# Performance work log

Hardware: AMD Instinct MI355X
Metric: run time of the kernel (lower is better)

## Reference

```python
import jax, jax.numpy as jnp
import numpy as np

H = 768; I = 3072; NH = 12; HD = H // NH; L = 2; V = 32000
N = 2048; NSUB = 8; SUBLEN = 256; WIDTH = 512; EPS = 1e-6


def rmsnorm(x, w):
    x32 = x.astype(jnp.float32)
    n = x32 * jax.lax.rsqrt(jnp.mean(x32 * x32, axis=-1, keepdims=True) + EPS)
    return (n * w).astype(x.dtype)


def fixed_pos_embedding(ages, dim):
    # inv_freq: [dim//2]; torch.linspace(0, 2, steps=dim//2)
    inv_freq = 1.0 / (10000.0 ** jnp.linspace(0.0, 2.0, dim // 2))
    t = ages[:, None] * inv_freq[None, :]              # [N, dim//2]
    # stack((s, s), -1).reshape -> duplicate each entry pairwise (interleaved)
    sin = jnp.repeat(jnp.sin(t), 2, axis=-1)[:, None, :]  # [N, 1, dim]
    cos = jnp.repeat(jnp.cos(t), 2, axis=-1)[:, None, :]
    return sin, cos


def apply_rope(x, sin, cos):
    # x: [N, heads, hd]; sin/cos: [N, 1, hd]
    x1 = x[..., 0::2]
    x2 = x[..., 1::2]
    rot = jnp.stack((-x2, x1), axis=-1).reshape(x.shape)
    return x * cos + rot * sin


def build_mask(subject_lengths, n):
    # block-diagonal (per subject) + causal local window of WIDTH
    csum = jnp.cumsum(subject_lengths)
    idx = jnp.arange(n)
    seg = jnp.searchsorted(csum, idx, side='right')   # subject id per token
    i = idx[:, None]; j = idx[None, :]
    same = seg[:, None] == seg[None, :]
    return same & (j <= i) & ((i - j) < WIDTH)        # [N, N] bool


def encoder_layer(x, time_data, sin, cos, mask, norm_w, W_in, W_out):
    h = rmsnorm(x, norm_w)
    all_time = jnp.concatenate((time_data, time_data ** 2), axis=-1)  # [N, 4]
    h = h.at[:, -all_time.shape[1]:].set(all_time.astype(h.dtype))
    t = h @ W_in                                      # [N, 2I + 3H]
    ff = t[:, : 2 * I]
    qkv = t[:, 2 * I:].reshape(-1, 3, NH, HD)
    q = apply_rope(qkv[:, 0], sin, cos)
    k = apply_rope(qkv[:, 1], sin, cos)
    v = qkv[:, 2]
    scores = jnp.einsum('qhd,khd->hqk', q, k) / jnp.sqrt(jnp.float32(HD))
    scores = jnp.where(mask[None, :, :], scores, -jnp.inf)
    probs = jax.nn.softmax(scores, axis=-1)
    attn = jnp.einsum('hqk,khd->qhd', probs, v).reshape(-1, H)
    x1, x2 = jnp.split(ff, 2, axis=-1)
    ffo = jax.nn.silu(x1) * x2                        # swiglu
    return jnp.concatenate((attn, ffo), axis=-1) @ W_out


def setup_inputs() -> dict:
    key = jax.random.key(0)
    ks = jax.random.split(key, 6)
    tokens = jax.random.randint(ks[0], (N,), 0, V)
    ages = jnp.sort(jax.random.uniform(ks[1], (N,), dtype=jnp.float32) * 100.0)
    time_data = jax.random.normal(ks[2], (N, 2), dtype=jnp.float32)
    subject_lengths = jnp.full((NSUB,), SUBLEN, dtype=jnp.int32)
    embed_table = jax.random.normal(ks[3], (V, H), dtype=jnp.float32) * 0.02
    in_norm_w = jnp.ones((H,), jnp.float32)
    out_norm_w = jnp.ones((H,), jnp.float32)
    layer_norm_w = jnp.ones((L, H), jnp.float32)
    layer_Win = jax.random.normal(ks[4], (L, H, 2 * I + 3 * H), dtype=jnp.float32) / np.sqrt(H)
    layer_Wout = jax.random.normal(ks[5], (L, H + I, H), dtype=jnp.float32) / np.sqrt(H + I)
    return dict(tokens=tokens, ages=ages, time_data=time_data,
                subject_lengths=subject_lengths, embed_table=embed_table,
                in_norm_w=in_norm_w, out_norm_w=out_norm_w,
                layer_norm_w=layer_norm_w, layer_Win=layer_Win, layer_Wout=layer_Wout)


def reference(tokens, ages, time_data, subject_lengths, embed_table,
              in_norm_w, out_norm_w, layer_norm_w, layer_Win, layer_Wout):
    x = embed_table[tokens]                           # [N, H]
    x = rmsnorm(x, in_norm_w)
    sin, cos = fixed_pos_embedding(ages, HD)
    mask = build_mask(subject_lengths, x.shape[0])
    for l in range(L):
        x = x + encoder_layer(x, time_data, sin, cos, mask,
                              layer_norm_w[l], layer_Win[l], layer_Wout[l])
    return rmsnorm(x, out_norm_w)
```

## Files before the change

### kernel.cpp

```cpp
#include <hip/hip_runtime.h>
#include <math.h>

typedef unsigned short ushort_t;
typedef float f32x4 __attribute__((ext_vector_type(4)));
typedef __bf16 bf16x8 __attribute__((ext_vector_type(8)));

#define DEVFN __device__ __forceinline__

DEVFN ushort_t f2bf(float f) {
  unsigned int u = __float_as_uint(f);
  u += 0x7FFFu + ((u >> 16) & 1u);
  return (ushort_t)(u >> 16);
}
DEVFN float bf2f(ushort_t u) { return __uint_as_float((unsigned int)u << 16); }

DEVFN void gload(const ushort_t* src, char* dst) {
  __builtin_amdgcn_global_load_lds(
      (const __attribute__((address_space(1))) unsigned int*)src,
      (__attribute__((address_space(3))) unsigned int*)dst, 16, 0, 0);
}

#define N_TOK  2048
#define HDIM   768
#define TCOLS  8448
#define FFI    3072
#define NHEADS 12
#define HD     64
#define NSEG   8
#define SEGLEN 256
#define ABCOLS 3840
#define NPART  6
#define KCHUNK 768

DEVFN void transpose_tile(const float* __restrict__ in, ushort_t* __restrict__ out,
                          int R, int C, int tr, int tc, int tid, char* smem) {
  ushort_t (*tile)[66] = (ushort_t(*)[66])smem;
  const int tx = tid & 31, ty = tid >> 5;
#pragma unroll
  for (int i = 0; i < 8; ++i) {
    const int r = ty + i * 8;
    tile[tx][r] = f2bf(in[(size_t)(tr + r) * C + tc + tx]);
  }
  __syncthreads();
#pragma unroll
  for (int i = 0; i < 4; ++i) {
    const int c = ty + i * 8;
    ushort2 pk; pk.x = tile[c][2 * tx]; pk.y = tile[c][2 * tx + 1];
    *(ushort2*)(out + (size_t)(tc + c) * R + tr + 2 * tx) = pk;
  }
}

__global__ __launch_bounds__(256) void preamble(
    const float* __restrict__ Win, ushort_t* __restrict__ winT,
    const float* __restrict__ embed, const int* __restrict__ tokens,
    const float* __restrict__ ages,
    const float* __restrict__ in_nw, const float* __restrict__ layer_nw,
    const float* __restrict__ time_data,
    float* __restrict__ x, ushort_t* __restrict__ hbuf, float2* __restrict__ sctab) {
  const int tid = threadIdx.x;
  if (blockIdx.x < 3168) {
    __shared__ char tsmem[32 * 66 * 2];
    const int id = blockIdx.x;
    transpose_tile(Win, winT, HDIM, TCOLS, (id / 264) * 64, (id % 264) * 32, tid, tsmem);
    return;
  }
  const int row = blockIdx.x - 3168;
  if (tid < 32) {
    const int k = tid;
    const float e = (2.0f * (float)k) / 31.0f;
    const float t = ages[row] * expf(-e * logf(10000.0f));
    float2 cs; cs.x = cosf(t); cs.y = sinf(t);
    sctab[row * HD + 2 * k] = cs;
    sctab[row * HD + 2 * k + 1] = cs;
  }
  __shared__ float part[4];
  const float* src = embed + (size_t)tokens[row] * HDIM;
  float4 v = {0.f, 0.f, 0.f, 0.f};
  const int c0 = tid * 4;
  if (tid < 192) v = *(const float4*)(src + c0);
  float ss = v.x * v.x + v.y * v.y + v.z * v.z + v.w * v.w;
#pragma unroll
  for (int off = 1; off < 64; off <<= 1) ss += __shfl_xor(ss, off);
  if ((tid & 63) == 0) part[tid >> 6] = ss;
  __syncthreads();
  const float rs = rsqrtf((part[0] + part[1] + part[2] + part[3]) * (1.0f / HDIM) + 1e-6f);
  float4 y = {0.f, 0.f, 0.f, 0.f};
  if (tid < 192) {
    y.x = v.x * rs * in_nw[c0]; y.y = v.y * rs * in_nw[c0 + 1];
    y.z = v.z * rs * in_nw[c0 + 2]; y.w = v.w * rs * in_nw[c0 + 3];
    *(float4*)(x + (size_t)row * HDIM + c0) = y;
  }
  float ss2 = y.x * y.x + y.y * y.y + y.z * y.z + y.w * y.w;
#pragma unroll
  for (int off = 1; off < 64; off <<= 1) ss2 += __shfl_xor(ss2, off);
  __syncthreads();
  if ((tid & 63) == 0) part[tid >> 6] = ss2;
  __syncthreads();
  const float rs2 = rsqrtf((part[0] + part[1] + part[2] + part[3]) * (1.0f / HDIM) + 1e-6f);
  if (tid < 192) {
    float val[4];
#pragma unroll
    for (int j = 0; j < 4; ++j) {
      const int c = c0 + j;
      float vv = ((const float*)&y)[j] * rs2 * layer_nw[c];
      if (c >= HDIM - 4) {
        const float td = time_data[row * 2 + (c & 1)];
        vv = (c >= HDIM - 2) ? td * td : td;
      }
      val[j] = vv;
    }
    ushort4 pk;
    pk.x = f2bf(val[0]); pk.y = f2bf(val[1]); pk.z = f2bf(val[2]); pk.w = f2bf(val[3]);
    *(ushort4*)(hbuf + (size_t)row * HDIM + c0) = pk;
  }
}

__global__ __launch_bounds__(256) void rms_fused(
    const ushort_t* __restrict__ cpartb, float* __restrict__ x,
    const float* __restrict__ w, const float* __restrict__ time_data,
    float* __restrict__ out_f32, ushort_t* __restrict__ out_bf16, const int mode) {
  const int row = blockIdx.x;
  const size_t stride = (size_t)N_TOK * HDIM;
  const int tid = threadIdx.x;
  const int c0 = tid * 4;
  float4 s = {0.f, 0.f, 0.f, 0.f};
  if (tid < 192) {
    s = *(const float4*)(x + (size_t)row * HDIM + c0);
#pragma unroll
    for (int z = 0; z < NPART; ++z) {
      const ushort4 p = *(const ushort4*)(cpartb + z * stride + (size_t)row * HDIM + c0);
      s.x += bf2f(p.x); s.y += bf2f(p.y); s.z += bf2f(p.z); s.w += bf2f(p.w);
    }
    if (mode == 1) *(float4*)(x + (size_t)row * HDIM + c0) = s;
  }
  float ss = s.x * s.x + s.y * s.y + s.z * s.z + s.w * s.w;
#pragma unroll
  for (int off = 1; off < 64; off <<= 1) ss += __shfl_xor(ss, off);
  __shared__ float part[4];
  if ((tid & 63) == 0) part[tid >> 6] = ss;
  __syncthreads();
  const float rs = rsqrtf((part[0] + part[1] + part[2] + part[3]) * (1.0f / HDIM) + 1e-6f);
  if (tid < 192) {
    float val[4];
#pragma unroll
    for (int j = 0; j < 4; ++j) {
      const int c = c0 + j;
      float vv = ((const float*)&s)[j] * rs * w[c];
      if (mode == 1 && c >= HDIM - 4) {
        const float td = time_data[row * 2 + (c & 1)];
        vv = (c >= HDIM - 2) ? td * td : td;
      }
      val[j] = vv;
    }
    if (mode == 1) {
      ushort4 pk;
      pk.x = f2bf(val[0]); pk.y = f2bf(val[1]); pk.z = f2bf(val[2]); pk.w = f2bf(val[3]);
      *(ushort4*)(out_bf16 + (size_t)row * HDIM + c0) = pk;
    } else {
      float4 o; o.x = val[0]; o.y = val[1]; o.z = val[2]; o.w = val[3];
      *(float4*)(out_f32 + (size_t)row * HDIM + c0) = o;
    }
  }
}

#define G1_NT 24
#define G1_ABYT 8192
#define G1_BUF  20480

DEVFN int swz64(int p) {
  const int g = ((p >> 6) & 3) ^ ((p >> 8) & 3);
  return p ^ (g << 4);
}
DEVFN int ffmap(int vr) {
  return (vr < 2 * FFI) ? ((((vr >> 4) & 1) * FFI) + ((vr >> 5) << 4) + (vr & 15)) : vr;
}

DEVFN void g1f_stage(const ushort_t* __restrict__ A, const ushort_t* __restrict__ BT,
                     int m0, int n0, int kt_el, char* buf, int tid) {
#pragma unroll
  for (int i = 0; i < 2; ++i) {
    const int q = swz64(i * 4096 + tid * 16);
    gload(A + (size_t)(m0 + (q >> 6)) * HDIM + kt_el + ((q & 63) >> 1),
          buf + i * 4096 + ((tid >> 6) << 10));
  }
#pragma unroll
  for (int i = 0; i < 3; ++i) {
    const int q = swz64(i * 4096 + tid * 16);
    const int vr = n0 + (q >> 6);
    gload(BT + (size_t)ffmap(vr) * HDIM + kt_el + ((q & 63) >> 1),
          buf + G1_ABYT + i * 4096 + ((tid >> 6) << 10));
  }
}

__global__ __launch_bounds__(256, 3) void gemm1f(
    const ushort_t* __restrict__ A, const ushort_t* __restrict__ BT,
    const float2* __restrict__ sctab,
    ushort_t* __restrict__ ab, ushort_t* __restrict__ qr,
    ushort_t* __restrict__ kr, ushort_t* __restrict__ vT,
    const float* __restrict__ tj1_src, ushort_t* __restrict__ tj1_dst,
    const float* __restrict__ tj2_src, ushort_t* __restrict__ tj2_dst) {
  __shared__ __align__(16) char smem[2 * G1_BUF];
  const int tid = threadIdx.x;
  const int bid = (int)blockIdx.x;
  if (bid >= 704) {
    int e = bid - 704;
    if (e < 1440)
      transpose_tile(tj1_src, tj1_dst, ABCOLS, HDIM, (e / 24) * 64, (e % 24) * 32, tid, smem);
    else {
      e -= 1440;
      transpose_tile(tj2_src, tj2_dst, HDIM, TCOLS, (e / 264) * 64, (e % 264) * 32, tid, smem);
    }
    return;
  }
  const int l = tid & 63, l15 = l & 15, l4 = l >> 4;
  const int wid = tid >> 6, wr = wid >> 1, wc = wid & 1;
  const int wg = (bid & 7) * 88 + (bid >> 3);
  const int nt = wg >> 4, mt = wg & 15;
  const int m0 = mt * 128, n0 = nt * 192;

  f32x4 acc[4][6] = {};

  g1f_stage(A, BT, m0, n0, 0,  smem, tid);
  g1f_stage(A, BT, m0, n0, 32, smem + G1_BUF, tid);
  asm volatile("s_waitcnt vmcnt(5)" ::: "memory");
  __builtin_amdgcn_s_barrier();
  __builtin_amdgcn_sched_barrier(0);

  for (int t = 0; t < G1_NT; ++t) {
    const char* bufA = smem + (t & 1) * G1_BUF;
    const char* bufB = bufA + G1_ABYT;
    bf16x8 a4[4], b6[6];
#pragma unroll
    for (int m = 0; m < 4; ++m) {
      const int p = (wr * 64 + m * 16 + l15) * 64 + l4 * 16;
      a4[m] = *(const bf16x8*)(bufA + swz64(p));
    }
#pragma unroll
    for (int n = 0; n < 6; ++n) {
      const int p = (wc * 96 + n * 16 + l15) * 64 + l4 * 16;
      b6[n] = *(const bf16x8*)(bufB + swz64(p));
    }
#pragma unroll
    for (int m = 0; m < 4; ++m)
#pragma unroll
      for (int n = 0; n < 6; ++n)
        acc[m][n] = __builtin_amdgcn_mfma_f32_16x16x32_bf16(a4[m], b6[n], acc[m][n], 0, 0, 0);

    if (t == G1_NT - 1) break;
    __builtin_amdgcn_sched_barrier(0);
    __builtin_amdgcn_s_barrier();
    if (t + 2 < G1_NT) {
      g1f_stage(A, BT, m0, n0, (t + 2) * 32, smem + (t & 1) * G1_BUF, tid);
      asm volatile("s_waitcnt vmcnt(5)" ::: "memory");
    } else {
      asm volatile("s_waitcnt vmcnt(0)" ::: "memory");
    }
    __builtin_amdgcn_s_barrier();
    __builtin_amdgcn_sched_barrier(0);
  }

  if (nt < 32) {
#pragma unroll
    for (int m = 0; m < 4; ++m)
#pragma unroll
      for (int np = 0; np < 3; ++np) {
        const int colj = (nt * 6 + wc * 3 + np) * 16 + l15;
#pragma unroll
        for (int r = 0; r < 4; ++r) {
          const float x1 = acc[m][2 * np][r], x2 = acc[m][2 * np + 1][r];
          const float sv = x1 / (1.f + __expf(-x1)) * x2;
          const int row = m0 + wr * 64 + m * 16 + l4 * 4 + r;
          ab[(size_t)row * ABCOLS + HDIM + colj] = f2bf(sv);
        }
      }
  } else {
#pragma unroll
    for (int n = 0; n < 6; ++n) {
      const int gcol = (nt - 32) * 192 + wc * 96 + n * 16;
      const int g = gcol >> 6;
      const int typ = g / NHEADS, h = g - typ * NHEADS;
      const int d = (gcol & 63) + l15;
      if (typ == 2) {
#pragma unroll
        for (int m = 0; m < 4; ++m) {
          ushort4 pk;
          pk.x = f2bf(acc[m][n][0]); pk.y = f2bf(acc[m][n][1]);
          pk.z = f2bf(acc[m][n][2]); pk.w = f2bf(acc[m][n][3]);
          const int row0 = m0 + wr * 64 + m * 16 + l4 * 4;
          *(ushort4*)(vT + ((size_t)h * HD + d) * N_TOK + row0) = pk;
        }
      } else {
        ushort_t* dst = (typ == 0) ? qr : kr;
        const float sgn = (l15 & 1) ? 1.f : -1.f;
#pragma unroll
        for (int m = 0; m < 4; ++m)
#pragma unroll
          for (int r = 0; r < 4; ++r) {
            const float val = acc[m][n][r];
            const float partner = __shfl_xor(val, 1);
            const int row = m0 + wr * 64 + m * 16 + l4 * 4 + r;
            const float2 cs = sctab[row * HD + d];
            dst[((size_t)h * N_TOK + row) * HD + d] = f2bf(val * cs.x + sgn * partner * cs.y);
          }
      }
    }
  }
}

#define G2_BUF 40960

DEVFN int swz128(int p) { return p ^ (((p >> 7) & 7) << 4); }

DEVFN void g2_stage(const ushort_t* __restrict__ A, const ushort_t* __restrict__ BT,
                    int m0, int n0, int kt_el, char* buf, int tid) {
#pragma unroll
  for (int i = 0; i < 10; ++i) {
    const int p = i * 4096 + tid * 16;
    const bool isA = p < 16384;
    const int q = swz128(isA ? p : p - 16384);
    const int row = q >> 7, colel = (q & 127) >> 1;
    const ushort_t* src = (isA ? A + (size_t)(m0 + row) * ABCOLS
                               : BT + (size_t)(n0 + row) * ABCOLS) + kt_el + colel;
    gload(src, buf + i * 4096 + ((tid >> 6) << 10));
  }
}

DEVFN void g2_body(const ushort_t* __restrict__ A, const ushort_t* __restrict__ BT,
                   char* smem, int m0, int n0, int kt0, int NT,
                   ushort_t* __restrict__ outp, int tid) {
  const int l = tid & 63, l15 = l & 15, l4 = l >> 4;
  const int w = tid >> 6, wr = w >> 1, wc = w & 1;
  f32x4 acc[4][6] = {};

  g2_stage(A, BT, m0, n0, kt0, smem, tid);
  g2_stage(A, BT, m0, n0, kt0 + 64, smem + G2_BUF, tid);
  asm volatile("s_waitcnt vmcnt(10)" ::: "memory");
  __builtin_amdgcn_s_barrier();
  __builtin_amdgcn_sched_barrier(0);

  for (int t = 0; t < NT; ++t) {
    const char* bufA = smem + (t & 1) * G2_BUF;
    const char* bufB = bufA + 16384;
#pragma unroll
    for (int kk = 0; kk < 2; ++kk) {
      bf16x8 af[4], bv[6];
#pragma unroll
      for (int mi = 0; mi < 4; ++mi) {
        const int p = (wr * 64 + mi * 16 + l15) * 128 + kk * 64 + l4 * 16;
        af[mi] = *(const bf16x8*)(bufA + swz128(p));
      }
#pragma unroll
      for (int ni = 0; ni < 6; ++ni) {
        const int p = (wc * 96 + ni * 16 + l15) * 128 + kk * 64 + l4 * 16;
        bv[ni] = *(const bf16x8*)(bufB + swz128(p));
      }
#pragma unroll
      for (int mi = 0; mi < 4; ++mi)
#pragma unroll
        for (int ni = 0; ni < 6; ++ni)
          acc[mi][ni] = __builtin_amdgcn_mfma_f32_16x16x32_bf16(af[mi], bv[ni], acc[mi][ni], 0, 0, 0);
    }

    if (t == NT - 1) break;
    __builtin_amdgcn_sched_barrier(0);
    __builtin_amdgcn_s_barrier();
    if (t + 2 < NT) {
      g2_stage(A, BT, m0, n0, kt0 + (t + 2) * 64, smem + (t & 1) * G2_BUF, tid);
      asm volatile("s_waitcnt vmcnt(10)" ::: "memory");
    } else {
      asm volatile("s_waitcnt vmcnt(0)" ::: "memory");
    }
    __builtin_amdgcn_s_barrier();
    __builtin_amdgcn_sched_barrier(0);
  }

#pragma unroll
  for (int mi = 0; mi < 4; ++mi)
#pragma unroll
    for (int ni = 0; ni < 6; ++ni)
#pragma unroll
      for (int r = 0; r < 4; ++r) {
        const int row = m0 + wr * 64 + mi * 16 + l4 * 4 + r;
        const int col = n0 + wc * 96 + ni * 16 + l15;
        outp[(size_t)row * HDIM + col] = f2bf(acc[mi][ni][r]);
      }
}

DEVFN void attn_one(const ushort_t* __restrict__ qr, const ushort_t* __restrict__ kr,
                    const ushort_t* __restrict__ vT, ushort_t* __restrict__ ab,
                    int h, int seg, int qt, ushort_t* Pw, int l15, int l4) {
  const int qrow0 = seg * SEGLEN + qt * 16;
  bf16x8 aq[2];
#pragma unroll
  for (int kk = 0; kk < 2; ++kk)
    aq[kk] = *(const bf16x8*)(qr + ((size_t)h * N_TOK + qrow0 + l15) * HD + kk * 32 + l4 * 8);

  f32x4 o[4] = {};
  float m_run[4], l_run[4];
#pragma unroll
  for (int r = 0; r < 4; ++r) { m_run[r] = -1e30f; l_run[r] = 0.f; }

  const int kbmax = qt >> 2;
  for (int kb = 0; kb <= kbmax; ++kb) {
    bf16x8 bk[4][2];
#pragma unroll
    for (int ni = 0; ni < 4; ++ni)
#pragma unroll
      for (int kk = 0; kk < 2; ++kk)
        bk[ni][kk] = *(const bf16x8*)(kr + ((size_t)h * N_TOK + seg * SEGLEN + kb * 64 + ni * 16 + l15) * HD + kk * 32 + l4 * 8);
    f32x4 s[4] = {};
#pragma unroll
    for (int ni = 0; ni < 4; ++ni)
#pragma unroll
      for (int kk = 0; kk < 2; ++kk)
        s[ni] = __builtin_amdgcn_mfma_f32_16x16x32_bf16(aq[kk], bk[ni][kk], s[ni], 0, 0, 0);

    const bool diag = (kb == kbmax);
#pragma unroll
    for (int ni = 0; ni < 4; ++ni)
#pragma unroll
      for (int r = 0; r < 4; ++r) {
        float v = s[ni][r] * 0.125f;
        if (diag) {
          const int qrow = qt * 16 + l4 * 4 + r;
          const int jcol = kb * 64 + ni * 16 + l15;
          if (jcol > qrow) v = -1e30f;
        }
        s[ni][r] = v;
      }

    float sc_[4];
#pragma unroll
    for (int r = 0; r < 4; ++r) {
      float pm = fmaxf(fmaxf(s[0][r], s[1][r]), fmaxf(s[2][r], s[3][r]));
      pm = fmaxf(pm, __shfl_xor(pm, 1));
      pm = fmaxf(pm, __shfl_xor(pm, 2));
      pm = fmaxf(pm, __shfl_xor(pm, 4));
      pm = fmaxf(pm, __shfl_xor(pm, 8));
      const float mn = fmaxf(m_run[r], pm);
      sc_[r] = __expf(m_run[r] - mn);
      m_run[r] = mn;
    }
#pragma unroll
    for (int ni = 0; ni < 4; ++ni)
#pragma unroll
      for (int r = 0; r < 4; ++r)
        s[ni][r] = __expf(s[ni][r] - m_run[r]);
#pragma unroll
    for (int r = 0; r < 4; ++r) {
      float ls = s[0][r] + s[1][r] + s[2][r] + s[3][r];
      ls += __shfl_xor(ls, 1);
      ls += __shfl_xor(ls, 2);
      ls += __shfl_xor(ls, 4);
      ls += __shfl_xor(ls, 8);
      l_run[r] = l_run[r] * sc_[r] + ls;
    }
#pragma unroll
    for (int ni = 0; ni < 4; ++ni)
#pragma unroll
      for (int r = 0; r < 4; ++r)
        o[ni][r] *= sc_[r];

#pragma unroll
    for (int ni = 0; ni < 4; ++ni)
#pragma unroll
      for (int r = 0; r < 4; ++r)
        Pw[(l4 * 4 + r) * 64 + ni * 16 + l15] = f2bf(s[ni][r]);

    bf16x8 pa[2], bv[4][2];
#pragma unroll
    for (int k2 = 0; k2 < 2; ++k2)
      pa[k2] = *(const bf16x8*)(&Pw[l15 * 64 + k2 * 32 + l4 * 8]);
#pragma unroll
    for (int ni = 0; ni < 4; ++ni)
#pragma unroll
      for (int k2 = 0; k2 < 2; ++k2)
        bv[ni][k2] = *(const bf16x8*)(vT + ((size_t)h * HD + ni * 16 + l15) * N_TOK + seg * SEGLEN + kb * 64 + k2 * 32 + l4 * 8);
#pragma unroll
    for (int ni = 0; ni < 4; ++ni)
#pragma unroll
      for (int k2 = 0; k2 < 2; ++k2)
        o[ni] = __builtin_amdgcn_mfma_f32_16x16x32_bf16(pa[k2], bv[ni][k2], o[ni], 0, 0, 0);
  }

#pragma unroll
  for (int ni = 0; ni < 4; ++ni)
#pragma unroll
    for (int r = 0; r < 4; ++r) {
      const int row = qrow0 + l4 * 4 + r;
      const int col = h * HD + ni * 16 + l15;
      ab[(size_t)row * ABCOLS + col] = f2bf(o[ni][r] / l_run[r]);
    }
}

__global__ __launch_bounds__(256, 2) void fused_mid(
    const ushort_t* __restrict__ ab, const ushort_t* __restrict__ woutT,
    ushort_t* __restrict__ cpartb,
    const ushort_t* __restrict__ qr, const ushort_t* __restrict__ kr,
    const ushort_t* __restrict__ vT, ushort_t* __restrict__ ab_out,
    const float* __restrict__ tj_src, ushort_t* __restrict__ tj_dst) {
  __shared__ __align__(16) char smem[2 * G2_BUF];
  const int b = (int)blockIdx.x;
  const int tid = threadIdx.x;
  if (b >= 448) {
    const int e = b - 448;
    transpose_tile(tj_src, tj_dst, ABCOLS, HDIM, (e / 24) * 64, (e % 24) * 32, tid, smem);
    return;
  }
  const int sel = b % 7;
  if (sel < 3) {
    const int a = (b / 7) * 3 + sel;
    const int h = a % NHEADS;
    const int r2 = a / NHEADS;
    const int seg = r2 & 7, p = r2 >> 3;
    const int w = tid >> 6, l = tid & 63;
    const int l15 = l & 15, l4 = l >> 4;
    ushort_t* Pw = (ushort_t*)smem + w * (16 * 64);
    attn_one(qr, kr, vT, ab_out, h, seg, p * 4 + w, Pw, l15, l4);
    attn_one(qr, kr, vT, ab_out, h, seg, (3 - p) * 4 + w, Pw, l15, l4);
  } else {
    const int f = (b / 7) * 4 + (sel - 3);
    const int z = 1 + (f >> 6);
    const int rem = f & 63;
    const int n0 = (rem & 3) * 192, m0 = (rem >> 2) * 128;
    g2_body(ab, woutT, smem, m0, n0, z * KCHUNK, 12,
            cpartb + (size_t)(z - 1) * N_TOK * HDIM, tid);
  }
}

__global__ __launch_bounds__(256, 2) void gemm2_z0(
    const ushort_t* __restrict__ ab, const ushort_t* __restrict__ woutT,
    ushort_t* __restrict__ cpartb) {
  __shared__ __align__(16) char smem[2 * G2_BUF];
  const int b = (int)blockIdx.x;
  const int half = b >> 6, rem = b & 63;
  const int n0 = (rem & 3) * 192, m0 = (rem >> 2) * 128;
  g2_body(ab, woutT, smem, m0, n0, half * 384, 6,
          cpartb + (size_t)(4 + half) * N_TOK * HDIM, threadIdx.x);
}

extern "C" void kernel_launch(void* const* d_in, const int* in_sizes, int n_in,
                              void* d_out, int out_size, void* d_ws, size_t ws_size,
                              hipStream_t stream) {
  const int*   tokens   = (const int*)d_in[0];
  const float* ages     = (const float*)d_in[1];
  const float* time_d   = (const float*)d_in[2];
  const float* embed    = (const float*)d_in[4];
  const float* in_nw    = (const float*)d_in[5];
  const float* out_nw   = (const float*)d_in[6];
  const float* layer_nw = (const float*)d_in[7];
  const float* Win      = (const float*)d_in[8];
  const float* Wout     = (const float*)d_in[9];
  float* out = (float*)d_out;

  char* ws = (char*)d_ws;
  float*    x      = (float*)   (ws + 0);
  ushort_t* hbuf   = (ushort_t*)(ws + 6291456);
  float2*   sctab  = (float2*)  (ws + 9437184);
  ushort_t* cpartb = (ushort_t*)(ws + 10485760);
  ushort_t* ab     = (ushort_t*)(ws + 29360128);
  ushort_t* qrb    = (ushort_t*)(ws + 45088768);
  ushort_t* krb    = (ushort_t*)(ws + 48234496);
  ushort_t* vTb    = (ushort_t*)(ws + 51380224);
  ushort_t* winT   = (ushort_t*)(ws + 54525952);
  ushort_t* woutT  = (ushort_t*)(ws + 80478208);

  const size_t winStride  = (size_t)TCOLS * HDIM;
  const size_t woutStride = (size_t)HDIM * ABCOLS;

  preamble<<<dim3(5216), dim3(256), 0, stream>>>(Win, winT, embed, tokens, ages,
                                                 in_nw, layer_nw, time_d, x, hbuf, sctab);

  for (int lyr = 0; lyr < 2; ++lyr) {
    if (lyr == 0) {
      gemm1f<<<dim3(704 + 4608), dim3(256), 0, stream>>>(
          hbuf, winT, sctab, ab, qrb, krb, vTb,
          Wout, woutT, Win + winStride, winT + winStride);
      fused_mid<<<dim3(448 + 1440), dim3(256), 0, stream>>>(
          ab, woutT, cpartb, qrb, krb, vTb, ab,
          Wout + woutStride, woutT + woutStride);
    } else {
      gemm1f<<<dim3(704), dim3(256), 0, stream>>>(
          hbuf, winT + winStride, sctab, ab, qrb, krb, vTb,
          nullptr, nullptr, nullptr, nullptr);
      fused_mid<<<dim3(448), dim3(256), 0, stream>>>(
          ab, woutT + woutStride, cpartb, qrb, krb, vTb, ab,
          nullptr, nullptr);
    }
    gemm2_z0<<<dim3(128), dim3(256), 0, stream>>>(ab, woutT + lyr * woutStride, cpartb);
    if (lyr == 0)
      rms_fused<<<dim3(N_TOK), dim3(256), 0, stream>>>(cpartb, x, layer_nw + HDIM, time_d,
                                                       nullptr, hbuf, 1);
    else
      rms_fused<<<dim3(N_TOK), dim3(256), 0, stream>>>(cpartb, x, out_nw, nullptr,
                                                       out, nullptr, 2);
  }
}
```

Before: 179.4 us.

## Load GEMM1 operands directly from global memory instead of LDS double-buffering

Removes the LDS staging pipeline (global_load_lds into swizzled double buffers, barriers and waitcnts) from the fused first GEMM. Each wave now reads its A and B fragments straight from global memory into registers through per-lane pointers that advance along K. The transpose path gets a small dedicated shared buffer. This drops barrier and LDS traffic and shrinks LDS use, but gives up data sharing between waves and the prefetch overlap, so global and L2 traffic rise and load latency is exposed.

```diff
diff --git a/kernel.cpp b/kernel.cpp
--- a/kernel.cpp
+++ b/kernel.cpp
@@ -164,32 +164,9 @@
 }
 
 #define G1_NT 24
-#define G1_ABYT 8192
-#define G1_BUF  20480
-
-DEVFN int swz64(int p) {
-  const int g = ((p >> 6) & 3) ^ ((p >> 8) & 3);
-  return p ^ (g << 4);
-}
+
 DEVFN int ffmap(int vr) {
   return (vr < 2 * FFI) ? ((((vr >> 4) & 1) * FFI) + ((vr >> 5) << 4) + (vr & 15)) : vr;
-}
-
-DEVFN void g1f_stage(const ushort_t* __restrict__ A, const ushort_t* __restrict__ BT,
-                     int m0, int n0, int kt_el, char* buf, int tid) {
-#pragma unroll
-  for (int i = 0; i < 2; ++i) {
-    const int q = swz64(i * 4096 + tid * 16);
-    gload(A + (size_t)(m0 + (q >> 6)) * HDIM + kt_el + ((q & 63) >> 1),
-          buf + i * 4096 + ((tid >> 6) << 10));
-  }
-#pragma unroll
-  for (int i = 0; i < 3; ++i) {
-    const int q = swz64(i * 4096 + tid * 16);
-    const int vr = n0 + (q >> 6);
-    gload(BT + (size_t)ffmap(vr) * HDIM + kt_el + ((q & 63) >> 1),
-          buf + G1_ABYT + i * 4096 + ((tid >> 6) << 10));
-  }
 }
 
 __global__ __launch_bounds__(256, 3) void gemm1f(
@@ -199,16 +176,16 @@
     ushort_t* __restrict__ kr, ushort_t* __restrict__ vT,
     const float* __restrict__ tj1_src, ushort_t* __restrict__ tj1_dst,
     const float* __restrict__ tj2_src, ushort_t* __restrict__ tj2_dst) {
-  __shared__ __align__(16) char smem[2 * G1_BUF];
+  __shared__ char tsmem[32 * 66 * 2];
   const int tid = threadIdx.x;
   const int bid = (int)blockIdx.x;
   if (bid >= 704) {
     int e = bid - 704;
     if (e < 1440)
-      transpose_tile(tj1_src, tj1_dst, ABCOLS, HDIM, (e / 24) * 64, (e % 24) * 32, tid, smem);
+      transpose_tile(tj1_src, tj1_dst, ABCOLS, HDIM, (e / 24) * 64, (e % 24) * 32, tid, tsmem);
     else {
       e -= 1440;
-      transpose_tile(tj2_src, tj2_dst, HDIM, TCOLS, (e / 264) * 64, (e % 264) * 32, tid, smem);
+      transpose_tile(tj2_src, tj2_dst, HDIM, TCOLS, (e / 264) * 64, (e % 264) * 32, tid, tsmem);
     }
     return;
   }
@@ -218,45 +195,30 @@
   const int nt = wg >> 4, mt = wg & 15;
   const int m0 = mt * 128, n0 = nt * 192;
 
+  const ushort_t* aptr[4];
+  const ushort_t* bptr[6];
+#pragma unroll
+  for (int m = 0; m < 4; ++m)
+    aptr[m] = A + (size_t)(m0 + wr * 64 + m * 16 + l15) * HDIM + l4 * 8;
+#pragma unroll
+  for (int n = 0; n < 6; ++n) {
+    const int vr = n0 + wc * 96 + n * 16 + l15;
+    bptr[n] = BT + (size_t)ffmap(vr) * HDIM + l4 * 8;
+  }
+
   f32x4 acc[4][6] = {};
 
-  g1f_stage(A, BT, m0, n0, 0,  smem, tid);
-  g1f_stage(A, BT, m0, n0, 32, smem + G1_BUF, tid);
-  asm volatile("s_waitcnt vmcnt(5)" ::: "memory");
-  __builtin_amdgcn_s_barrier();
-  __builtin_amdgcn_sched_barrier(0);
-
   for (int t = 0; t < G1_NT; ++t) {
-    const char* bufA = smem + (t & 1) * G1_BUF;
-    const char* bufB = bufA + G1_ABYT;
     bf16x8 a4[4], b6[6];
 #pragma unroll
-    for (int m = 0; m < 4; ++m) {
-      const int p = (wr * 64 + m * 16 + l15) * 64 + l4 * 16;
-      a4[m] = *(const bf16x8*)(bufA + swz64(p));
-    }
-#pragma unroll
-    for (int n = 0; n < 6; ++n) {
-      const int p = (wc * 96 + n * 16 + l15) * 64 + l4 * 16;
-      b6[n] = *(const bf16x8*)(bufB + swz64(p));
-    }
+    for (int m = 0; m < 4; ++m) { a4[m] = *(const bf16x8*)aptr[m]; aptr[m] += 32; }
+#pragma unroll
+    for (int n = 0; n < 6; ++n) { b6[n] = *(const bf16x8*)bptr[n]; bptr[n] += 32; }
 #pragma unroll
     for (int m = 0; m < 4; ++m)
 #pragma unroll
       for (int n = 0; n < 6; ++n)
         acc[m][n] = __builtin_amdgcn_mfma_f32_16x16x32_bf16(a4[m], b6[n], acc[m][n], 0, 0, 0);
-
-    if (t == G1_NT - 1) break;
-    __builtin_amdgcn_sched_barrier(0);
-    __builtin_amdgcn_s_barrier();
-    if (t + 2 < G1_NT) {
-      g1f_stage(A, BT, m0, n0, (t + 2) * 32, smem + (t & 1) * G1_BUF, tid);
-      asm volatile("s_waitcnt vmcnt(5)" ::: "memory");
-    } else {
-      asm volatile("s_waitcnt vmcnt(0)" ::: "memory");
-    }
-    __builtin_amdgcn_s_barrier();
-    __builtin_amdgcn_sched_barrier(0);
   }
 
   if (nt < 32) {
```

Result: slower. 286.5 us (+59.7%).
